# Performance work log

Hardware: AMD Instinct MI355X
Metric: run time of the kernel (lower is better)

## Reference

```python
import jax, jax.numpy as jnp
import numpy as np

N_NODES = 100000
N_EDGES = 1600000
F = 64          # node_features (in == out for EvolveGCNO)
HID = 64        # hidden_size


def setup_inputs() -> dict:
    key = jax.random.key(0)
    ks = jax.random.split(key, 12)
    s = 1.0 / np.sqrt(F)
    inp = {
        "x": jax.random.normal(ks[0], (N_NODES, F), dtype=jnp.float32),
        "edge_index": jax.random.randint(ks[1], (2, N_EDGES), 0, N_NODES, dtype=jnp.int64),
        "edge_weight": jax.random.uniform(ks[2], (N_EDGES,), dtype=jnp.float32),
        # evolving GCN weight (initial_weight of EvolveGCNO)
        "W0": jax.random.uniform(ks[3], (F, F), jnp.float32, -s, s),
        # GRU (input_size=F, hidden_size=F): gates ordered r, z, n
        "gru_Wi": jax.random.uniform(ks[4], (3 * F, F), jnp.float32, -s, s),
        "gru_Wh": jax.random.uniform(ks[5], (3 * F, F), jnp.float32, -s, s),
        "gru_bi": jax.random.uniform(ks[6], (3 * F,), jnp.float32, -s, s),
        "gru_bh": jax.random.uniform(ks[7], (3 * F,), jnp.float32, -s, s),
        # projection F -> HID and head HID -> 1
        "proj_W": jax.random.uniform(ks[8], (HID, F), jnp.float32, -s, s),
        "proj_b": jax.random.uniform(ks[9], (HID,), jnp.float32, -s, s),
        "lin_W": jax.random.uniform(ks[10], (1, HID), jnp.float32, -1.0 / np.sqrt(HID), 1.0 / np.sqrt(HID)),
        "lin_b": jax.random.uniform(ks[11], (1,), jnp.float32, -1.0 / np.sqrt(HID), 1.0 / np.sqrt(HID)),
    }
    return inp


def reference(x, edge_index, edge_weight, W0, gru_Wi, gru_Wh, gru_bi, gru_bh,
              proj_W, proj_b, lin_W, lin_b):
    N = x.shape[0]
    # --- EvolveGCNO weight evolution: one GRU step, rows of W0 are both input and hidden ---
    gi = W0 @ gru_Wi.T + gru_bi  # [F, 3F]
    gh = W0 @ gru_Wh.T + gru_bh  # [F, 3F]
    i_r, i_z, i_n = jnp.split(gi, 3, axis=1)
    h_r, h_z, h_n = jnp.split(gh, 3, axis=1)
    r = jax.nn.sigmoid(i_r + h_r)
    z = jax.nn.sigmoid(i_z + h_z)
    n = jnp.tanh(i_n + r * h_n)
    W = (1.0 - z) * n + z * W0  # evolved GCN weight [F, F]

    # --- GCNConv with fixed evolved W: X' = D^-1/2 (A + I) D^-1/2 (X W) ---
    xw = x @ W  # [N, F]
    src, dst = edge_index[0], edge_index[1]
    loop = jnp.arange(N)
    src2 = jnp.concatenate([src, loop])
    dst2 = jnp.concatenate([dst, loop])
    w2 = jnp.concatenate([edge_weight, jnp.ones((N,), xw.dtype)])  # self-loop weight 1
    deg = jax.ops.segment_sum(w2, dst2, num_segments=N)
    dinv = jnp.where(deg > 0, jax.lax.rsqrt(deg), 0.0)
    norm = dinv[src2] * w2 * dinv[dst2]  # [E + N]
    h = jax.ops.segment_sum(xw[src2] * norm[:, None], dst2, num_segments=N)  # [N, F]

    # --- MLP head (dropout is identity in eval) ---
    h = jax.nn.relu(h @ proj_W.T + proj_b)
    return h @ lin_W.T + lin_b  # [N, 1]
```

## Files before the change

### kernel.cpp

```cpp
#include <hip/hip_runtime.h>
#include <stdint.h>

#define FDIM 64
#define BINSH 6
#define NBINS 1563
#define BCAP 1536
#define OVCAP 8192
#define PSTAGE 4096

__global__ __launch_bounds__(256) void k_sentinel(float* out, int N, float val) {
    int n = blockIdx.x * 256 + threadIdx.x;
    if (n < N) out[n] = (n == 0) ? val : 0.f;
}

__global__ __launch_bounds__(64) void k_evolve(
    const float* __restrict__ W0, const float* __restrict__ Wi,
    const float* __restrict__ Wh, const float* __restrict__ bi,
    const float* __restrict__ bh, float* __restrict__ W) {
    int i = blockIdx.x;
    int j = threadIdx.x;
    __shared__ float w0s[64];
    w0s[j] = W0[i * 64 + j];
    __syncthreads();
    float a0 = 0.f, a1 = 0.f, a2 = 0.f, b0 = 0.f, b1 = 0.f, b2 = 0.f;
#pragma unroll 8
    for (int k = 0; k < 64; k++) {
        float w0k = w0s[k];
        a0 += w0k * Wi[(j)       * 64 + k];
        a1 += w0k * Wi[(64 + j)  * 64 + k];
        a2 += w0k * Wi[(128 + j) * 64 + k];
        b0 += w0k * Wh[(j)       * 64 + k];
        b1 += w0k * Wh[(64 + j)  * 64 + k];
        b2 += w0k * Wh[(128 + j) * 64 + k];
    }
    float ir = a0 + bi[j],        hr = b0 + bh[j];
    float iz = a1 + bi[64 + j],   hz = b1 + bh[64 + j];
    float in_ = a2 + bi[128 + j], hn = b2 + bh[128 + j];
    float r = 1.f / (1.f + expf(-(ir + hr)));
    float z = 1.f / (1.f + expf(-(iz + hz)));
    float n = tanhf(in_ + r * hn);
    W[i * 64 + j] = (1.f - z) * n + z * w0s[j];
}

__global__ __launch_bounds__(64) void k_matM(
    const float* __restrict__ W, const float* __restrict__ projW,
    float* __restrict__ MT) {
    int k = blockIdx.x;
    int j = threadIdx.x;
    __shared__ float wr[64];
    wr[j] = W[k * 64 + j];
    __syncthreads();
    float s = 0.f;
#pragma unroll 8
    for (int q = 0; q < 64; q++) s += wr[q] * projW[j * 64 + q];
    MT[j * 64 + k] = s;
}

__global__ __launch_bounds__(1024) void k_part(
    const int* __restrict__ src, const int* __restrict__ dst,
    const float* __restrict__ ew, int* __restrict__ gcnt,
    int2* __restrict__ part, int* __restrict__ ovf_cnt,
    int* __restrict__ ovs, int* __restrict__ ovd, float* __restrict__ ovw,
    int E) {
    __shared__ int  hist[NBINS];
    __shared__ int  scn[NBINS];
    __shared__ int  lcur[NBINS];
    __shared__ int2 stage[PSTAGE];
    __shared__ unsigned short sbin[PSTAGE];
    int t = threadIdx.x;
    for (int b = t; b < NBINS; b += 1024) hist[b] = 0;
    __syncthreads();
    int e0 = blockIdx.x * PSTAGE;
    int cnt = E - e0; if (cnt > PSTAGE) cnt = PSTAGE;
    for (int i = t; i < cnt; i += 1024) atomicAdd(&hist[dst[e0 + i] >> BINSH], 1);
    __syncthreads();
    for (int b = t; b < NBINS; b += 1024) scn[b] = hist[b];
    __syncthreads();
    for (int off = 1; off < NBINS; off <<= 1) {
        int i1 = t, i2 = t + 1024;
        int a1 = (i1 < NBINS && i1 >= off) ? scn[i1 - off] : 0;
        int a2 = (i2 < NBINS && i2 >= off) ? scn[i2 - off] : 0;
        __syncthreads();
        if (i1 < NBINS) scn[i1] += a1;
        if (i2 < NBINS) scn[i2] += a2;
        __syncthreads();
    }
    for (int b = t; b < NBINS; b += 1024) {
        int h = hist[b];
        int lbase = scn[b] - h;
        int gb = h ? atomicAdd(&gcnt[b], h) : 0;
        lcur[b] = lbase;
        hist[b] = gb - lbase;
    }
    __syncthreads();
    for (int i = t; i < cnt; i += 1024) {
        int e = e0 + i;
        int d = dst[e];
        int b = d >> BINSH;
        int p = atomicAdd(&lcur[b], 1);
        stage[p] = make_int2(src[e] | ((d & 63) << 20), __float_as_int(ew[e]));
        sbin[p] = (unsigned short)b;
    }
    __syncthreads();
    for (int i = t; i < cnt; i += 1024) {
        int b = sbin[i];
        int2 e = stage[i];
        int p = i + hist[b];
        if (p < BCAP) {
            part[(size_t)b * BCAP + p] = e;
        } else {
            int op = atomicAdd(ovf_cnt, 1);
            if (op < OVCAP) {
                ovs[op] = e.x & 0xFFFFF;
                ovd[op] = (b << BINSH) | ((e.x >> 20) & 63);
                ovw[op] = __int_as_float(e.y);
            }
        }
    }
}

__global__ __launch_bounds__(256) void k_deg2(
    const int* __restrict__ gcnt, const int2* __restrict__ part,
    const int* __restrict__ ovf_cnt, const int* __restrict__ ovd,
    const float* __restrict__ ovw,
    float* __restrict__ deg, float* __restrict__ dinv, int N) {
    __shared__ float dl[64];
    int t = threadIdx.x, b = blockIdx.x;
    if (t < 64) dl[t] = 1.0f;
    __syncthreads();
    int c = gcnt[b]; if (c > BCAP) c = BCAP;
    const int2* pe = part + (size_t)b * BCAP;
    for (int i = t; i < c; i += 256) {
        int2 e = pe[i];
        atomicAdd(&dl[(e.x >> 20) & 63], __int_as_float(e.y));
    }
    int m = *ovf_cnt; if (m > OVCAP) m = OVCAP;
    for (int i = t; i < m; i += 256) {
        int d = ovd[i];
        if ((d >> BINSH) == b) atomicAdd(&dl[d & 63], ovw[i]);
    }
    __syncthreads();
    int n = b * 64 + t;
    if (t < 64 && n < N) {
        float d = dl[t];
        deg[n] = d;
        dinv[n] = d > 0.f ? rsqrtf(d) : 0.f;
    }
}

__global__ __launch_bounds__(256) void k_gather2(
    const float* __restrict__ x, const float* __restrict__ dinv,
    const int* __restrict__ gcnt, const int2* __restrict__ part,
    float* __restrict__ agg, int N) {
    __shared__ int  lcnt[64];
    __shared__ int  loff[65];
    __shared__ int  lcur[64];
    __shared__ int2 ledge[BCAP];
    int t = threadIdx.x, b = blockIdx.x;
    if (t < 64) lcnt[t] = 0;
    __syncthreads();
    int c = gcnt[b]; if (c > BCAP) c = BCAP;
    const int2* pe = part + (size_t)b * BCAP;
    for (int i = t; i < c; i += 256) {
        atomicAdd(&lcnt[(pe[i].x >> 20) & 63], 1);
    }
    __syncthreads();
    if (t == 0) {
        int o = 0;
#pragma unroll 16
        for (int k = 0; k < 64; k++) { loff[k] = o; o += lcnt[k]; }
        loff[64] = o;
    }
    __syncthreads();
    if (t < 64) lcur[t] = loff[t];
    __syncthreads();
    for (int i = t; i < c; i += 256) {
        int2 e = pe[i];
        int s = e.x & 0xFFFFF;
        float nw = dinv[s] * __int_as_float(e.y);
        int p = atomicAdd(&lcur[(e.x >> 20) & 63], 1);
        ledge[p] = make_int2(e.x, __float_as_int(nw));
    }
    __syncthreads();
    int wv = t >> 6, lane = t & 63, eg = lane >> 4, f = (lane & 15) * 4;
    for (int nl = wv; nl < 64; nl += 4) {
        int n = b * 64 + nl;
        if (n >= N) continue;
        float dn = dinv[n];
        int beg = loff[nl], end = loff[nl + 1];
        float ax = 0.f, ay = 0.f, az = 0.f, aw = 0.f;
        float bx = 0.f, by = 0.f, bz = 0.f, bw = 0.f;
        int i = beg + eg;
        for (; i + 4 < end; i += 8) {
            int2 e0 = ledge[i];
            int2 e1 = ledge[i + 4];
            int s0 = e0.x & 0xFFFFF, s1 = e1.x & 0xFFFFF;
            float4 v0 = *(const float4*)&x[(size_t)s0 * 64 + f];
            float4 v1 = *(const float4*)&x[(size_t)s1 * 64 + f];
            float nm0 = __int_as_float(e0.y);
            float nm1 = __int_as_float(e1.y);
            ax += nm0 * v0.x; ay += nm0 * v0.y; az += nm0 * v0.z; aw += nm0 * v0.w;
            bx += nm1 * v1.x; by += nm1 * v1.y; bz += nm1 * v1.z; bw += nm1 * v1.w;
        }
        for (; i < end; i += 4) {
            int2 e = ledge[i];
            int s = e.x & 0xFFFFF;
            float nm = __int_as_float(e.y);
            float4 xv = *(const float4*)&x[(size_t)s * 64 + f];
            ax += nm * xv.x; ay += nm * xv.y; az += nm * xv.z; aw += nm * xv.w;
        }
        ax += bx; ay += by; az += bz; aw += bw;
        ax *= dn; ay *= dn; az *= dn; aw *= dn;
        ax += __shfl_xor(ax, 16); ay += __shfl_xor(ay, 16);
        az += __shfl_xor(az, 16); aw += __shfl_xor(aw, 16);
        ax += __shfl_xor(ax, 32); ay += __shfl_xor(ay, 32);
        az += __shfl_xor(az, 32); aw += __shfl_xor(aw, 32);
        if (eg == 0) {
            float sl = dn * dn;
            float4 xv = *(const float4*)&x[(size_t)n * 64 + f];
            float4 o = make_float4(ax + sl * xv.x, ay + sl * xv.y,
                                   az + sl * xv.z, aw + sl * xv.w);
            *(float4*)&agg[(size_t)n * 64 + f] = o;
        }
    }
}

__global__ __launch_bounds__(256) void k_head(
    const float* __restrict__ agg, const float* __restrict__ MT,
    const float* __restrict__ projB, const float* __restrict__ linW,
    const float* __restrict__ linB, const float* __restrict__ x,
    const float* __restrict__ dinv, const int* __restrict__ ovf_cnt,
    const int* __restrict__ ovs, const int* __restrict__ ovd,
    const float* __restrict__ ovw, float* __restrict__ out, int N) {
    __shared__ float hs[64 * 68];
    __shared__ float ps[64 * 68];
    __shared__ float red[64 * 17];
    __shared__ float pbs[64], lws[64];
    int t  = threadIdx.x;
    int nb = blockIdx.x * 64;
#pragma unroll
    for (int i = 0; i < 4; i++) {
        int lin = i * 1024 + t * 4;
        int row = lin >> 6, col = lin & 63;
        int node = nb + row;
        float4 v = make_float4(0.f, 0.f, 0.f, 0.f);
        if (node < N) v = *(const float4*)(agg + (size_t)node * 64 + col);
        *(float4*)&hs[row * 68 + col] = v;
        *(float4*)&ps[row * 68 + col] = *(const float4*)(MT + lin);
    }
    if (t < 64) { pbs[t] = projB[t]; lws[t] = linW[t]; }
    __syncthreads();
    int m = *ovf_cnt; if (m > OVCAP) m = OVCAP;
    for (int i = t; i < m; i += 256) {
        int d = ovd[i];
        if ((d >> BINSH) == blockIdx.x && d < N) {
            int s = ovs[i];
            float nm = dinv[s] * ovw[i] * dinv[d];
            int nl = d & 63;
            for (int ff = 0; ff < 64; ff++)
                atomicAdd(&hs[nl * 68 + ff], nm * x[(size_t)s * 64 + ff]);
        }
    }
    if (m) __syncthreads();
    int tj = t & 15, tn = t >> 4;
    float acc[4][4] = {};
    for (int k = 0; k < 64; k += 4) {
        float4 hv[4], pv[4];
#pragma unroll
        for (int nn = 0; nn < 4; nn++) hv[nn] = *(const float4*)&hs[(tn * 4 + nn) * 68 + k];
#pragma unroll
        for (int jj = 0; jj < 4; jj++) pv[jj] = *(const float4*)&ps[(tj * 4 + jj) * 68 + k];
#pragma unroll
        for (int nn = 0; nn < 4; nn++) {
            const float* hp = (const float*)&hv[nn];
#pragma unroll
            for (int jj = 0; jj < 4; jj++) {
                const float* pp = (const float*)&pv[jj];
                acc[nn][jj] += hp[0] * pp[0] + hp[1] * pp[1] + hp[2] * pp[2] + hp[3] * pp[3];
            }
        }
    }
    float lb = linB[0];
#pragma unroll
    for (int nn = 0; nn < 4; nn++) {
        float s = 0.f;
#pragma unroll
        for (int jj = 0; jj < 4; jj++) {
            int j = tj * 4 + jj;
            float v = acc[nn][jj] + pbs[j];
            v = v > 0.f ? v : 0.f;
            s += v * lws[j];
        }
        red[(tn * 4 + nn) * 17 + tj] = s;
    }
    __syncthreads();
    if (t < 64) {
        float s = lb;
#pragma unroll
        for (int q = 0; q < 16; q++) s += red[t * 17 + q];
        int node = nb + t;
        if (node < N) out[node] = s;
    }
}

extern "C" void kernel_launch(void* const* d_in, const int* in_sizes, int n_in,
                              void* d_out, int out_size, void* d_ws, size_t ws_size,
                              hipStream_t stream) {
    const float* x   = (const float*)d_in[0];
    const int*   ei  = (const int*)d_in[1];
    const float* ew  = (const float*)d_in[2];
    const float* W0  = (const float*)d_in[3];
    const float* gWi = (const float*)d_in[4];
    const float* gWh = (const float*)d_in[5];
    const float* gbi = (const float*)d_in[6];
    const float* gbh = (const float*)d_in[7];
    const float* pW  = (const float*)d_in[8];
    const float* pb  = (const float*)d_in[9];
    const float* lW  = (const float*)d_in[10];
    const float* lb  = (const float*)d_in[11];
    float* out = (float*)d_out;

    static const int EXPSZ[12] = {6400000, 3200000, 1600000, 4096, 12288, 12288,
                                  192, 192, 4096, 64, 64, 1};
    int mism = -1;
    for (int i = 0; i < 12 && i < n_in; i++)
        if (in_sizes[i] != EXPSZ[i]) { mism = i; break; }
    if (mism >= 0) {
        k_sentinel<<<(out_size + 255) / 256, 256, 0, stream>>>(out, out_size,
                                                               ldexpf(1.f, 30 + 3 * mism));
        return;
    }

    int N = in_sizes[0] / FDIM;
    int E = in_sizes[1] / 2;
    const int* src = ei;
    const int* dst = ei + E;

    char* wsb = (char*)d_ws;
    float* W       = (float*)(wsb);
    float* MT      = (float*)(wsb + (16u << 10));
    int*   gcnt    = (int*)  (wsb + (32u << 10));
    int*   ovf_cnt = (int*)  (wsb + (39u << 10));
    int*   ovs     = (int*)  (wsb + (44u << 10));
    int*   ovd     = (int*)  (wsb + (76u << 10));
    float* ovw     = (float*)(wsb + (108u << 10));
    float* deg     = (float*)(wsb + (512u << 10));
    float* dinv    = (float*)(wsb + (1u << 20));
    int2*  part    = (int2*) (wsb + (2u << 20));
    float* agg     = (float*)(wsb + (22u << 20));

    hipMemsetAsync(gcnt, 0, (8u << 10), stream);

    k_evolve<<<64, 64, 0, stream>>>(W0, gWi, gWh, gbi, gbh, W);
    k_matM<<<64, 64, 0, stream>>>(W, pW, MT);
    k_part<<<(E + PSTAGE - 1) / PSTAGE, 1024, 0, stream>>>(src, dst, ew, gcnt, part,
                                                           ovf_cnt, ovs, ovd, ovw, E);
    k_deg2<<<NBINS, 256, 0, stream>>>(gcnt, part, ovf_cnt, ovd, ovw, deg, dinv, N);
    k_gather2<<<NBINS, 256, 0, stream>>>(x, dinv, gcnt, part, agg, N);
    k_head<<<NBINS, 256, 0, stream>>>(agg, MT, pb, lW, lb, x, dinv,
                                      ovf_cnt, ovs, ovd, ovw, out, N);
}
```

Measured before the change: 225.2 us.

## Premultiply x by fused weight, gather bf16 rows, fuse head into gather

```diff
diff --git a/kernel.cpp b/kernel.cpp
--- a/kernel.cpp
+++ b/kernel.cpp
@@ -7,6 +7,16 @@
 #define BCAP 1536
 #define OVCAP 8192
 #define PSTAGE 4096
+
+__device__ __forceinline__ float bf2f(unsigned int u) {
+    union { float f; uint32_t i; } v; v.i = (u & 0xFFFFu) << 16; return v.f;
+}
+__device__ __forceinline__ unsigned short f2bf(float f) {
+    union { float f; uint32_t i; } v; v.f = f;
+    uint32_t u = v.i;
+    u += 0x7FFFu + ((u >> 16) & 1u);
+    return (unsigned short)(u >> 16);
+}
 
 __global__ __launch_bounds__(256) void k_sentinel(float* out, int N, float val) {
     int n = blockIdx.x * 256 + threadIdx.x;
@@ -44,7 +54,7 @@
 
 __global__ __launch_bounds__(64) void k_matM(
     const float* __restrict__ W, const float* __restrict__ projW,
-    float* __restrict__ MT) {
+    float* __restrict__ M) {
     int k = blockIdx.x;
     int j = threadIdx.x;
     __shared__ float wr[64];
@@ -53,7 +63,59 @@
     float s = 0.f;
 #pragma unroll 8
     for (int q = 0; q < 64; q++) s += wr[q] * projW[j * 64 + q];
-    MT[j * 64 + k] = s;
+    M[k * 64 + j] = s;
+}
+
+__global__ __launch_bounds__(256) void k_xm(
+    const float* __restrict__ x, const float* __restrict__ M,
+    unsigned short* __restrict__ xm, int N) {
+    __shared__ float xs[64 * 68];
+    __shared__ float ms[64 * 68];
+    int t  = threadIdx.x;
+    int nb = blockIdx.x * 64;
+#pragma unroll
+    for (int i = 0; i < 4; i++) {
+        int lin = i * 1024 + t * 4;
+        int row = lin >> 6, col = lin & 63;
+        int node = nb + row;
+        float4 v = make_float4(0.f, 0.f, 0.f, 0.f);
+        if (node < N) v = *(const float4*)(x + (size_t)node * 64 + col);
+        *(float4*)&xs[row * 68 + col] = v;
+        *(float4*)&ms[row * 68 + col] = *(const float4*)(M + lin);
+    }
+    __syncthreads();
+    int tj = t & 15, tn = t >> 4;
+    float acc[4][4] = {};
+    for (int k = 0; k < 64; k += 4) {
+        float4 xv[4], mv[4];
+#pragma unroll
+        for (int nn = 0; nn < 4; nn++) xv[nn] = *(const float4*)&xs[(tn * 4 + nn) * 68 + k];
+#pragma unroll
+        for (int kk = 0; kk < 4; kk++) mv[kk] = *(const float4*)&ms[(k + kk) * 68 + tj * 4];
+#pragma unroll
+        for (int nn = 0; nn < 4; nn++) {
+            const float* xp = (const float*)&xv[nn];
+#pragma unroll
+            for (int kk = 0; kk < 4; kk++) {
+                float xk = xp[kk];
+                const float* mp = (const float*)&mv[kk];
+                acc[nn][0] += xk * mp[0];
+                acc[nn][1] += xk * mp[1];
+                acc[nn][2] += xk * mp[2];
+                acc[nn][3] += xk * mp[3];
+            }
+        }
+    }
+#pragma unroll
+    for (int nn = 0; nn < 4; nn++) {
+        int node = nb + tn * 4 + nn;
+        if (node < N) {
+            ushort4 o;
+            o.x = f2bf(acc[nn][0]); o.y = f2bf(acc[nn][1]);
+            o.z = f2bf(acc[nn][2]); o.w = f2bf(acc[nn][3]);
+            *(ushort4*)&xm[(size_t)node * 64 + tj * 4] = o;
+        }
+    }
 }
 
 __global__ __launch_bounds__(1024) void k_part(
@@ -148,16 +210,20 @@
     }
 }
 
-__global__ __launch_bounds__(256) void k_gather2(
-    const float* __restrict__ x, const float* __restrict__ dinv,
+__global__ __launch_bounds__(256) void k_gf(
+    const unsigned short* __restrict__ xm, const float* __restrict__ dinv,
     const int* __restrict__ gcnt, const int2* __restrict__ part,
-    float* __restrict__ agg, int N) {
+    const float* __restrict__ projB, const float* __restrict__ linW,
+    const float* __restrict__ linB, const int* __restrict__ ovf_cnt,
+    const int* __restrict__ ovs, const int* __restrict__ ovd,
+    const float* __restrict__ ovw, float* __restrict__ out, int N) {
     __shared__ int  lcnt[64];
     __shared__ int  loff[65];
     __shared__ int  lcur[64];
     __shared__ int2 ledge[BCAP];
+    __shared__ float pbs[64], lws[64];
     int t = threadIdx.x, b = blockIdx.x;
-    if (t < 64) lcnt[t] = 0;
+    if (t < 64) { lcnt[t] = 0; pbs[t] = projB[t]; lws[t] = linW[t]; }
     __syncthreads();
     int c = gcnt[b]; if (c > BCAP) c = BCAP;
     const int2* pe = part + (size_t)b * BCAP;
@@ -182,7 +248,9 @@
         ledge[p] = make_int2(e.x, __float_as_int(nw));
     }
     __syncthreads();
-    int wv = t >> 6, lane = t & 63, eg = lane >> 4, f = (lane & 15) * 4;
+    int m = *ovf_cnt; if (m > OVCAP) m = OVCAP;
+    float lb = linB[0];
+    int wv = t >> 6, lane = t & 63, eg = lane >> 4, fq = lane & 15, f = fq * 4;
     for (int nl = wv; nl < 64; nl += 4) {
         int n = b * 64 + nl;
         if (n >= N) continue;
@@ -195,19 +263,22 @@
             int2 e0 = ledge[i];
             int2 e1 = ledge[i + 4];
             int s0 = e0.x & 0xFFFFF, s1 = e1.x & 0xFFFFF;
-            float4 v0 = *(const float4*)&x[(size_t)s0 * 64 + f];
-            float4 v1 = *(const float4*)&x[(size_t)s1 * 64 + f];
+            uint2 u0 = *(const uint2*)&xm[(size_t)s0 * 64 + f];
+            uint2 u1 = *(const uint2*)&xm[(size_t)s1 * 64 + f];
             float nm0 = __int_as_float(e0.y);
             float nm1 = __int_as_float(e1.y);
-            ax += nm0 * v0.x; ay += nm0 * v0.y; az += nm0 * v0.z; aw += nm0 * v0.w;
-            bx += nm1 * v1.x; by += nm1 * v1.y; bz += nm1 * v1.z; bw += nm1 * v1.w;
+            ax += nm0 * bf2f(u0.x);       ay += nm0 * bf2f(u0.x >> 16);
+            az += nm0 * bf2f(u0.y);       aw += nm0 * bf2f(u0.y >> 16);
+            bx += nm1 * bf2f(u1.x);       by += nm1 * bf2f(u1.x >> 16);
+            bz += nm1 * bf2f(u1.y);       bw += nm1 * bf2f(u1.y >> 16);
         }
         for (; i < end; i += 4) {
             int2 e = ledge[i];
             int s = e.x & 0xFFFFF;
             float nm = __int_as_float(e.y);
-            float4 xv = *(const float4*)&x[(size_t)s * 64 + f];
-            ax += nm * xv.x; ay += nm * xv.y; az += nm * xv.z; aw += nm * xv.w;
+            uint2 u = *(const uint2*)&xm[(size_t)s * 64 + f];
+            ax += nm * bf2f(u.x); ay += nm * bf2f(u.x >> 16);
+            az += nm * bf2f(u.y); aw += nm * bf2f(u.y >> 16);
         }
         ax += bx; ay += by; az += bz; aw += bw;
         ax *= dn; ay *= dn; az *= dn; aw *= dn;
@@ -216,90 +287,31 @@
         ax += __shfl_xor(ax, 32); ay += __shfl_xor(ay, 32);
         az += __shfl_xor(az, 32); aw += __shfl_xor(aw, 32);
         if (eg == 0) {
-            float sl = dn * dn;
-            float4 xv = *(const float4*)&x[(size_t)n * 64 + f];
-            float4 o = make_float4(ax + sl * xv.x, ay + sl * xv.y,
-                                   az + sl * xv.z, aw + sl * xv.w);
-            *(float4*)&agg[(size_t)n * 64 + f] = o;
-        }
-    }
-}
-
-__global__ __launch_bounds__(256) void k_head(
-    const float* __restrict__ agg, const float* __restrict__ MT,
-    const float* __restrict__ projB, const float* __restrict__ linW,
-    const float* __restrict__ linB, const float* __restrict__ x,
-    const float* __restrict__ dinv, const int* __restrict__ ovf_cnt,
-    const int* __restrict__ ovs, const int* __restrict__ ovd,
-    const float* __restrict__ ovw, float* __restrict__ out, int N) {
-    __shared__ float hs[64 * 68];
-    __shared__ float ps[64 * 68];
-    __shared__ float red[64 * 17];
-    __shared__ float pbs[64], lws[64];
-    int t  = threadIdx.x;
-    int nb = blockIdx.x * 64;
-#pragma unroll
-    for (int i = 0; i < 4; i++) {
-        int lin = i * 1024 + t * 4;
-        int row = lin >> 6, col = lin & 63;
-        int node = nb + row;
-        float4 v = make_float4(0.f, 0.f, 0.f, 0.f);
-        if (node < N) v = *(const float4*)(agg + (size_t)node * 64 + col);
-        *(float4*)&hs[row * 68 + col] = v;
-        *(float4*)&ps[row * 68 + col] = *(const float4*)(MT + lin);
-    }
-    if (t < 64) { pbs[t] = projB[t]; lws[t] = linW[t]; }
-    __syncthreads();
-    int m = *ovf_cnt; if (m > OVCAP) m = OVCAP;
-    for (int i = t; i < m; i += 256) {
-        int d = ovd[i];
-        if ((d >> BINSH) == blockIdx.x && d < N) {
-            int s = ovs[i];
-            float nm = dinv[s] * ovw[i] * dinv[d];
-            int nl = d & 63;
-            for (int ff = 0; ff < 64; ff++)
-                atomicAdd(&hs[nl * 68 + ff], nm * x[(size_t)s * 64 + ff]);
-        }
-    }
-    if (m) __syncthreads();
-    int tj = t & 15, tn = t >> 4;
-    float acc[4][4] = {};
-    for (int k = 0; k < 64; k += 4) {
-        float4 hv[4], pv[4];
-#pragma unroll
-        for (int nn = 0; nn < 4; nn++) hv[nn] = *(const float4*)&hs[(tn * 4 + nn) * 68 + k];
-#pragma unroll
-        for (int jj = 0; jj < 4; jj++) pv[jj] = *(const float4*)&ps[(tj * 4 + jj) * 68 + k];
-#pragma unroll
-        for (int nn = 0; nn < 4; nn++) {
-            const float* hp = (const float*)&hv[nn];
-#pragma unroll
-            for (int jj = 0; jj < 4; jj++) {
-                const float* pp = (const float*)&pv[jj];
-                acc[nn][jj] += hp[0] * pp[0] + hp[1] * pp[1] + hp[2] * pp[2] + hp[3] * pp[3];
+            {
+                uint2 u = *(const uint2*)&xm[(size_t)n * 64 + f];
+                float sl = dn * dn;
+                ax += sl * bf2f(u.x); ay += sl * bf2f(u.x >> 16);
+                az += sl * bf2f(u.y); aw += sl * bf2f(u.y >> 16);
             }
-        }
-    }
-    float lb = linB[0];
-#pragma unroll
-    for (int nn = 0; nn < 4; nn++) {
-        float s = 0.f;
-#pragma unroll
-        for (int jj = 0; jj < 4; jj++) {
-            int j = tj * 4 + jj;
-            float v = acc[nn][jj] + pbs[j];
-            v = v > 0.f ? v : 0.f;
-            s += v * lws[j];
-        }
-        red[(tn * 4 + nn) * 17 + tj] = s;
-    }
-    __syncthreads();
-    if (t < 64) {
-        float s = lb;
-#pragma unroll
-        for (int q = 0; q < 16; q++) s += red[t * 17 + q];
-        int node = nb + t;
-        if (node < N) out[node] = s;
+            for (int q = 0; q < m; q++) {
+                if (ovd[q] == n) {
+                    int s = ovs[q];
+                    float nm = dinv[s] * ovw[q] * dn;
+                    uint2 u = *(const uint2*)&xm[(size_t)s * 64 + f];
+                    ax += nm * bf2f(u.x); ay += nm * bf2f(u.x >> 16);
+                    az += nm * bf2f(u.y); aw += nm * bf2f(u.y >> 16);
+                }
+            }
+            float v0 = ax + pbs[f],     v1 = ay + pbs[f + 1];
+            float v2 = az + pbs[f + 2], v3 = aw + pbs[f + 3];
+            float s = (v0 > 0.f ? v0 : 0.f) * lws[f]
+                    + (v1 > 0.f ? v1 : 0.f) * lws[f + 1]
+                    + (v2 > 0.f ? v2 : 0.f) * lws[f + 2]
+                    + (v3 > 0.f ? v3 : 0.f) * lws[f + 3];
+            s += __shfl_xor(s, 1); s += __shfl_xor(s, 2);
+            s += __shfl_xor(s, 4); s += __shfl_xor(s, 8);
+            if (fq == 0) out[n] = s + lb;
+        }
     }
 }
 
@@ -338,7 +350,7 @@
 
     char* wsb = (char*)d_ws;
     float* W       = (float*)(wsb);
-    float* MT      = (float*)(wsb + (16u << 10));
+    float* M       = (float*)(wsb + (16u << 10));
     int*   gcnt    = (int*)  (wsb + (32u << 10));
     int*   ovf_cnt = (int*)  (wsb + (39u << 10));
     int*   ovs     = (int*)  (wsb + (44u << 10));
@@ -347,16 +359,16 @@
     float* deg     = (float*)(wsb + (512u << 10));
     float* dinv    = (float*)(wsb + (1u << 20));
     int2*  part    = (int2*) (wsb + (2u << 20));
-    float* agg     = (float*)(wsb + (22u << 20));
+    unsigned short* xm = (unsigned short*)(wsb + (22u << 20));
 
     hipMemsetAsync(gcnt, 0, (8u << 10), stream);
 
     k_evolve<<<64, 64, 0, stream>>>(W0, gWi, gWh, gbi, gbh, W);
-    k_matM<<<64, 64, 0, stream>>>(W, pW, MT);
+    k_matM<<<64, 64, 0, stream>>>(W, pW, M);
+    k_xm<<<NBINS, 256, 0, stream>>>(x, M, xm, N);
     k_part<<<(E + PSTAGE - 1) / PSTAGE, 1024, 0, stream>>>(src, dst, ew, gcnt, part,
                                                            ovf_cnt, ovs, ovd, ovw, E);
     k_deg2<<<NBINS, 256, 0, stream>>>(gcnt, part, ovf_cnt, ovd, ovw, deg, dinv, N);
-    k_gather2<<<NBINS, 256, 0, stream>>>(x, dinv, gcnt, part, agg, N);
-    k_head<<<NBINS, 256, 0, stream>>>(agg, MT, pb, lW, lb, x, dinv,
-                                      ovf_cnt, ovs, ovd, ovw, out, N);
-}
+    k_gf<<<NBINS, 256, 0, stream>>>(xm, dinv, gcnt, part, pb, lW, lb,
+                                    ovf_cnt, ovs, ovd, ovw, out, N);
+}
```

New measurement: 206.6 us. 1.09x faster.
